# Performance work log

Measured on AMD Instinct MI355X. Metric: run time of the kernel, lower is better.

Reference implementation:

```python
import jax, jax.numpy as jnp
import numpy as np

C, H, V, N, T = 1024, 256, 10000, 16, 256


def setup_inputs() -> dict:
    key = jax.random.key(0)
    ks = jax.random.split(key, 16)
    s = 1.0 / np.sqrt(H)
    rn = lambda k, shape, sc: (jax.random.normal(k, shape, dtype=jnp.float32) * sc)
    d = {}
    d["text"] = jax.random.randint(ks[0], (N, T), 0, V)
    d["start_emb"] = rn(ks[1], (C, H), 1.0)
    d["sw1"] = rn(ks[2], (H, H), s); d["sb1"] = jnp.zeros((H,), jnp.float32)
    d["sw2"] = rn(ks[3], (H, H), s); d["sb2"] = jnp.zeros((H,), jnp.float32)
    d["sw3"] = rn(ks[4], (H, 1), s); d["sb3"] = jnp.zeros((1,), jnp.float32)
    d["state_emb"] = rn(ks[5], (C, H), 1.0)
    d["tw1"] = rn(ks[6], (H, H), s); d["tb1"] = jnp.zeros((H,), jnp.float32)
    d["tw2"] = rn(ks[7], (H, H), s); d["tb2"] = jnp.zeros((H,), jnp.float32)
    d["tw3"] = rn(ks[8], (H, C), s); d["tb3"] = jnp.zeros((C,), jnp.float32)
    d["pre_emb"] = rn(ks[9], (C, H), 1.0)
    d["ew1"] = rn(ks[10], (H, H), s); d["eb1"] = jnp.zeros((H,), jnp.float32)
    d["ew2"] = rn(ks[11], (H, H), s); d["eb2"] = jnp.zeros((H,), jnp.float32)
    d["ew3"] = rn(ks[12], (H, V), s); d["eb3"] = jnp.zeros((V,), jnp.float32)
    return d


def _res(x, w1, b1, w2, b2):
    # ResidualLayerOld: relu(lin2(relu(lin1(x)))) + x
    return jax.nn.relu(jax.nn.relu(x @ w1 + b1) @ w2 + b2) + x


def reference(text, start_emb, sw1, sb1, sw2, sb2, sw3, sb3,
              state_emb, tw1, tb1, tw2, tb2, tw3, tb3,
              pre_emb, ew1, eb1, ew2, eb2, ew3, eb3):
    # start: [C] log p(z_0)
    start = jax.nn.log_softmax((_res(start_emb, sw1, sb1, sw2, sb2) @ sw3 + sb3)[:, 0])
    # transition: log_softmax over next state, then permute -> [next, prev]
    trans = jax.nn.log_softmax(_res(state_emb, tw1, tb1, tw2, tb2) @ tw3 + tb3, axis=-1).T
    # emission: log_softmax over vocab, permute -> [V, C]
    emit = jax.nn.log_softmax(_res(pre_emb, ew1, eb1, ew2, eb2) @ ew3 + eb3, axis=-1).T

    obs = emit[text]                      # [N, T, C] log p(x_t | z_t=c)
    alpha0 = start[None, :] + obs[:, 0]   # [N, C]

    def step(alpha, e_t):
        # log-semiring matvec: alpha'[n,j] = logsumexp_i alpha[n,i] + trans[j,i]
        a = jax.scipy.special.logsumexp(alpha[:, None, :] + trans[None, :, :], axis=-1) + e_t
        return a, None

    alpha, _ = jax.lax.scan(step, alpha0, jnp.swapaxes(obs, 0, 1)[1:])
    # evidence: logsumexp over final states, summed over batch (full lengths)
    return jax.scipy.special.logsumexp(alpha, axis=-1).sum()
```

## Files before the change

### kernel.cpp

```cpp
#include <hip/hip_runtime.h>
#include <hip/hip_bf16.h>
#include <cstddef>

#define CC 1024
#define HH 256
#define VV 10000
#define NN 16
#define TT 256
#define NB 16
#define NVB 40

typedef __attribute__((ext_vector_type(8))) short s8b;
typedef __attribute__((ext_vector_type(4))) float f32x4;
typedef __attribute__((ext_vector_type(4))) unsigned int u32x4;

__device__ __forceinline__ unsigned short f2bf(float f) {
    unsigned int b = __builtin_bit_cast(unsigned int, f);
    b += 0x7FFFu + ((b >> 16) & 1u);
    return (unsigned short)(b >> 16);
}
__device__ __forceinline__ float bf2f(unsigned short u) {
    return __builtin_bit_cast(float, ((unsigned int)u) << 16);
}

struct ResArgs { const float *x, *w1, *b1, *w2, *b2; float* o; };
struct ResArgs3 { ResArgs a[3]; };

__global__ __launch_bounds__(256) void k_res(ResArgs3 A)
{
    ResArgs R = A.a[blockIdx.y];
    const int r0 = blockIdx.x * 16;
    const int th = threadIdx.x;
    __shared__ float xs[256][24];
    __shared__ float hs[256][24];
    #pragma unroll
    for (int k = 0; k < 16; k++) xs[th][k] = R.x[(size_t)(r0 + k) * HH + th];
    __syncthreads();
    float acc[16];
    float b1v = R.b1[th];
    #pragma unroll
    for (int r = 0; r < 16; r++) acc[r] = b1v;
    for (int h = 0; h < HH; h++) {
        float w = R.w1[(size_t)h * HH + th];
        #pragma unroll
        for (int r = 0; r < 16; r++) acc[r] = fmaf(xs[h][r], w, acc[r]);
    }
    #pragma unroll
    for (int r = 0; r < 16; r++) hs[th][r] = fmaxf(acc[r], 0.f);
    __syncthreads();
    float b2v = R.b2[th];
    #pragma unroll
    for (int r = 0; r < 16; r++) acc[r] = b2v;
    for (int h = 0; h < HH; h++) {
        float w = R.w2[(size_t)h * HH + th];
        #pragma unroll
        for (int r = 0; r < 16; r++) acc[r] = fmaf(hs[h][r], w, acc[r]);
    }
    #pragma unroll
    for (int r = 0; r < 16; r++) {
        size_t idx = (size_t)(r0 + r) * HH + th;
        R.o[idx] = fmaxf(acc[r], 0.f) + R.x[idx];
    }
}

__global__ __launch_bounds__(256) void k_slog(const float* __restrict__ res_s,
                                              const float* __restrict__ sw3,
                                              const float* __restrict__ sb3,
                                              float* __restrict__ slog)
{
    __shared__ float wv[256];
    const int th = threadIdx.x;
    const int c = blockIdx.x * 256 + th;
    wv[th] = sw3[th];
    __syncthreads();
    const float* row = res_s + (size_t)c * HH;
    float acc = 0.f;
    for (int h = 0; h < HH; h++) acc = fmaf(row[h], wv[h], acc);
    slog[c] = acc + sb3[0];
}

__global__ __launch_bounds__(256) void k_pt(const float* __restrict__ res_t,
                                            const float* __restrict__ tw3,
                                            const float* __restrict__ tb3,
                                            unsigned short* __restrict__ PB)
{
    const int r0 = blockIdx.x * 4;
    const int th = threadIdx.x;
    __shared__ float rs[4][256];
    __shared__ float sred[256];
    for (int k = 0; k < 4; k++) rs[k][th] = res_t[(size_t)(r0 + k) * HH + th];
    __syncthreads();
    float acc[4][4];
    #pragma unroll
    for (int r = 0; r < 4; r++)
        #pragma unroll
        for (int q = 0; q < 4; q++) acc[r][q] = tb3[th + q * 256];
    for (int h = 0; h < HH; h++) {
        float w0 = tw3[(size_t)h * CC + th];
        float w1 = tw3[(size_t)h * CC + th + 256];
        float w2 = tw3[(size_t)h * CC + th + 512];
        float w3 = tw3[(size_t)h * CC + th + 768];
        #pragma unroll
        for (int r = 0; r < 4; r++) {
            float xv = rs[r][h];
            acc[r][0] = fmaf(xv, w0, acc[r][0]);
            acc[r][1] = fmaf(xv, w1, acc[r][1]);
            acc[r][2] = fmaf(xv, w2, acc[r][2]);
            acc[r][3] = fmaf(xv, w3, acc[r][3]);
        }
    }
    for (int r = 0; r < 4; r++) {
        float m = fmaxf(fmaxf(acc[r][0], acc[r][1]), fmaxf(acc[r][2], acc[r][3]));
        sred[th] = m; __syncthreads();
        for (int off = 128; off > 0; off >>= 1) { if (th < off) sred[th] = fmaxf(sred[th], sred[th + off]); __syncthreads(); }
        float rm = sred[0]; __syncthreads();
        float ssum = __expf(acc[r][0] - rm) + __expf(acc[r][1] - rm) + __expf(acc[r][2] - rm) + __expf(acc[r][3] - rm);
        sred[th] = ssum; __syncthreads();
        for (int off = 128; off > 0; off >>= 1) { if (th < off) sred[th] += sred[th + off]; __syncthreads(); }
        float inv = 1.0f / sred[0]; __syncthreads();
        #pragma unroll
        for (int q = 0; q < 4; q++) {
            float p = __expf(acc[r][q] - rm) * inv;
            PB[(size_t)(th + q * 256) * CC + (r0 + r)] = f2bf(p);
        }
    }
}

__global__ __launch_bounds__(256) void k_emitg(const float* __restrict__ res_e,
                                               const float* __restrict__ ew3,
                                               const float* __restrict__ eb3,
                                               unsigned short* __restrict__ emitT,
                                               float* __restrict__ epart2)
{
    const int vb = blockIdx.x, c0 = blockIdx.y * 64;
    const int th = threadIdx.x;
    const int w = th >> 6, l = th & 63;
    const int lhi = l >> 4, llo = l & 15;
    const int wv = w & 1, wc = w >> 1;

    __shared__ __align__(16) unsigned short ewT[64 * 256];
    __shared__ __align__(16) unsigned short rsb[64 * 256];
    __shared__ float ebl[64];
    __shared__ float wlse[4][2][16][2];

    {
        char* base = (char*)rsb;
        #pragma unroll
        for (int i = 0; i < 8; i++) {
            int g = i * 2048 + th * 8;
            int row = g >> 8, h0 = g & 255;
            const float* src = res_e + (size_t)(c0 + row) * HH + h0;
            float4 f0 = *(const float4*)(src);
            float4 f1 = *(const float4*)(src + 4);
            s8b pk;
            pk[0] = (short)f2bf(f0.x); pk[1] = (short)f2bf(f0.y);
            pk[2] = (short)f2bf(f0.z); pk[3] = (short)f2bf(f0.w);
            pk[4] = (short)f2bf(f1.x); pk[5] = (short)f2bf(f1.y);
            pk[6] = (short)f2bf(f1.z); pk[7] = (short)f2bf(f1.w);
            *(s8b*)(base + row * 512 + ((h0 * 2) ^ ((row & 7) << 4))) = pk;
        }
    }

    float rM[2] = {-1e30f, -1e30f}, rS[2] = {0.f, 0.f};

    for (int r = 0; r < 4; r++) {
        const int v0r = vb * 256 + r * 64;
        __syncthreads();
        {
            int tv = th & 63;
            char* base = (char*)ewT;
            int rowoff = tv * 512;
            int key = (tv & 7) << 4;
            int vglob = v0r + tv;
            bool valid = vglob < VV;
            #pragma unroll 8
            for (int i = 0; i < 64; i++) {
                int h = (th >> 6) + i * 4;
                float x = valid ? ew3[(size_t)h * VV + vglob] : 0.f;
                *(unsigned short*)(base + rowoff + ((h * 2) ^ key)) = f2bf(x);
            }
        }
        if (th < 64) ebl[th] = (v0r + th < VV) ? eb3[v0r + th] : 0.f;
        __syncthreads();

        f32x4 acc[2][2] = {{{0,0,0,0},{0,0,0,0}},{{0,0,0,0},{0,0,0,0}}};
        const char* ea = (const char*)ewT;
        const char* rb = (const char*)rsb;
        const int arow0 = wv * 32 + llo, arow1 = wv * 32 + 16 + llo;
        const int brow0 = wc * 32 + llo, brow1 = wc * 32 + 16 + llo;
        const int akey0 = (arow0 & 7) << 4, akey1 = akey0;
        const int bkey0 = (brow0 & 7) << 4;
        #pragma unroll
        for (int kt = 0; kt < 8; kt++) {
            int off = kt * 64 + lhi * 16;
            s8b a0 = *(const s8b*)(ea + arow0 * 512 + (off ^ akey0));
            s8b a1 = *(const s8b*)(ea + arow1 * 512 + (off ^ akey1));
            s8b b0 = *(const s8b*)(rb + brow0 * 512 + (off ^ bkey0));
            s8b b1 = *(const s8b*)(rb + brow1 * 512 + (off ^ bkey0));
            acc[0][0] = __builtin_amdgcn_mfma_f32_16x16x32_bf16(a0, b0, acc[0][0], 0, 0, 0);
            acc[0][1] = __builtin_amdgcn_mfma_f32_16x16x32_bf16(a0, b1, acc[0][1], 0, 0, 0);
            acc[1][0] = __builtin_amdgcn_mfma_f32_16x16x32_bf16(a1, b0, acc[1][0], 0, 0, 0);
            acc[1][1] = __builtin_amdgcn_mfma_f32_16x16x32_bf16(a1, b1, acc[1][1], 0, 0, 0);
        }

        float um[2] = {-1e30f, -1e30f}, us[2] = {0.f, 0.f};
        #pragma unroll
        for (int u = 0; u < 2; u++) {
            float vals[8];
            #pragma unroll
            for (int s = 0; s < 2; s++) {
                #pragma unroll
                for (int q = 0; q < 4; q++) {
                    int vloc = wv * 32 + s * 16 + lhi * 4 + q;
                    int vglob = v0r + vloc;
                    float logit = acc[s][u][q] + ebl[vloc];
                    bool valid = vglob < VV;
                    if (valid)
                        emitT[(size_t)vglob * CC + (c0 + wc * 32 + u * 16 + llo)] = f2bf(logit);
                    vals[s * 4 + q] = valid ? logit : -1e30f;
                }
            }
            float m = vals[0];
            #pragma unroll
            for (int e = 1; e < 8; e++) m = fmaxf(m, vals[e]);
            float ss = 0.f;
            #pragma unroll
            for (int e = 0; e < 8; e++) ss += __expf(vals[e] - m);
            #pragma unroll
            for (int o = 16; o < 64; o <<= 1) {
                float m2 = __shfl_xor(m, o);
                float s2 = __shfl_xor(ss, o);
                float nm = fmaxf(m, m2);
                ss = ss * __expf(m - nm) + s2 * __expf(m2 - nm);
                m = nm;
            }
            um[u] = m; us[u] = ss;
        }
        if (l < 16) {
            #pragma unroll
            for (int u = 0; u < 2; u++) {
                wlse[w][u][l][0] = um[u];
                wlse[w][u][l][1] = us[u];
            }
        }
        __syncthreads();
        if (th < 64) {
            int wc2 = th >> 5, u2 = (th >> 4) & 1, ll2 = th & 15;
            float m1 = wlse[2 * wc2][u2][ll2][0], s1 = wlse[2 * wc2][u2][ll2][1];
            float m2 = wlse[2 * wc2 + 1][u2][ll2][0], s2 = wlse[2 * wc2 + 1][u2][ll2][1];
            float nm = fmaxf(m1, m2);
            float ns = s1 * __expf(m1 - nm) + s2 * __expf(m2 - nm);
            float om = rM[0], os = rS[0];
            float fm = fmaxf(om, nm);
            rS[0] = os * __expf(om - fm) + ns * __expf(nm - fm);
            rM[0] = fm;
        }
    }
    if (th < 64) {
        epart2[((size_t)vb * CC + c0 + th) * 2]     = rM[0];
        epart2[((size_t)vb * CC + c0 + th) * 2 + 1] = rS[0];
    }
}

__global__ __launch_bounds__(256) void k_lse(const float* __restrict__ epart2,
                                             float* __restrict__ lse)
{
    int c = blockIdx.x * 256 + threadIdx.x;
    float M = -1e30f, S = 0.f;
    for (int vb = 0; vb < NVB; vb++) {
        float m  = epart2[((size_t)vb * CC + c) * 2];
        float s2 = epart2[((size_t)vb * CC + c) * 2 + 1];
        float nm = fmaxf(M, m);
        S = S * __expf(M - nm) + s2 * __expf(m - nm);
        M = nm;
    }
    lse[c] = M + __logf(S);
}

__global__ __launch_bounds__(256) void k_eprob(unsigned short* __restrict__ emitT,
                                               const float* __restrict__ lse)
{
    __shared__ float ls[1024];
    const int th = threadIdx.x;
    for (int i = th; i < 1024; i += 256) ls[i] = lse[i];
    __syncthreads();
    size_t base = ((size_t)blockIdx.x * 256 + th) * 8;
    int c0 = (int)(base & 1023);
    s8b v = *(const s8b*)(emitT + base);
    unsigned short o[8];
    #pragma unroll
    for (int e = 0; e < 8; e++)
        o[e] = f2bf(__expf(bf2f((unsigned short)v[e]) - ls[c0 + e]));
    s8b ov;
    #pragma unroll
    for (int e = 0; e < 8; e++) ov[e] = (short)o[e];
    *(s8b*)(emitT + base) = ov;
}

__device__ __forceinline__ void load_stage(const unsigned short* vbuf_t, int th, char* vl)
{
    const unsigned short* sb = vbuf_t + th * 8;
    s8b ch[8];
    #pragma unroll
    for (int c = 0; c < 8; c++)
        asm volatile("global_load_dwordx4 %0, %1, off sc0 sc1"
                     : "=v"(ch[c]) : "v"(sb + c * 2048));
    asm volatile("s_waitcnt vmcnt(0)" ::: "memory");
    __builtin_amdgcn_sched_barrier(0);
    for (;;) {
        unsigned int miss = 0u;
        #pragma unroll
        for (int c = 0; c < 8; c++) {
            u32x4 d = __builtin_bit_cast(u32x4, ch[c]);
            if (d[0] == 0xFFFFFFFFu || d[1] == 0xFFFFFFFFu ||
                d[2] == 0xFFFFFFFFu || d[3] == 0xFFFFFFFFu) miss |= 1u << c;
        }
        if (miss == 0u) break;
        #pragma unroll
        for (int c = 0; c < 8; c++)
            if (miss & (1u << c))
                asm volatile("global_load_dwordx4 %0, %1, off sc0 sc1"
                             : "=v"(ch[c]) : "v"(sb + c * 2048));
        asm volatile("s_waitcnt vmcnt(0)" ::: "memory");
        __builtin_amdgcn_sched_barrier(0);
    }
    #pragma unroll
    for (int c = 0; c < 8; c++) {
        int ow = c * 4096 + th * 16;
        *(s8b*)(vl + (ow ^ (((ow >> 11) & 7) << 4))) = ch[c];
    }
}

__global__ void __launch_bounds__(256, 1) k_fwd(
    const unsigned short* __restrict__ PB,
    const unsigned short* __restrict__ eprob,
    const float* __restrict__ slog,
    const int* __restrict__ text,
    unsigned short* vbuf,
    float* __restrict__ outp)
{
    const int blk = blockIdx.x;
    const int th = threadIdx.x;
    const int w = th >> 6, l = th & 63;
    const int lhi = l >> 4, llo = l & 15;
    const int jglob = blk * 64 + w * 16 + llo;

    __shared__ int toks[NN * TT];
    __shared__ __align__(16) unsigned short vlds[NN * CC];
    __shared__ __align__(16) unsigned short vtile[16][72];
    __shared__ float swk[4];
    __shared__ float fin[16];

    for (int i = th; i < NN * TT; i += 256) toks[i] = text[i];

    s8b bfr[32];
    {
        const unsigned short* pbj = PB + (size_t)jglob * CC + lhi * 8;
        #pragma unroll
        for (int kt = 0; kt < 32; kt++)
            bfr[kt] = *(const s8b*)(pbj + kt * 32);
    }
    s8b ones;
    #pragma unroll
    for (int e = 0; e < 8; e++) ones[e] = (short)0x3F80;

    float x0 = slog[th], x1 = slog[th + 256], x2 = slog[th + 512], x3 = slog[th + 768];
    float mw = fmaxf(fmaxf(x0, x1), fmaxf(x2, x3));
    #pragma unroll
    for (int o = 32; o; o >>= 1) mw = fmaxf(mw, __shfl_xor(mw, o));
    __syncthreads();
    if (l == 0) swk[w] = mw;
    __syncthreads();
    float gm = fmaxf(fmaxf(swk[0], swk[1]), fmaxf(swk[2], swk[3]));
    __syncthreads();
    float e4 = __expf(x0 - gm) + __expf(x1 - gm) + __expf(x2 - gm) + __expf(x3 - gm);
    #pragma unroll
    for (int o = 32; o; o >>= 1) e4 += __shfl_xor(e4, o);
    if (l == 0) swk[w] = e4;
    __syncthreads();
    float slse = gm + __logf(swk[0] + swk[1] + swk[2] + swk[3]);
    __syncthreads();

    if (th < 64) {
        int jj = blk * 64 + th;
        float p0 = __expf(slog[jj] - slse);
        #pragma unroll
        for (int n = 0; n < 16; n++)
            vtile[n][th] = f2bf(p0 * bf2f(eprob[(size_t)toks[n * TT] * CC + jj]));
    }
    __syncthreads();
    if (th < 128) {
        int n = th >> 3, seg = th & 7;
        s8b val = *(const s8b*)&vtile[n][seg * 8];
        unsigned short* dst = vbuf + (size_t)n * CC + blk * 64 + seg * 8;
        asm volatile("global_store_dwordx4 %0, %1, off sc0 sc1" :: "v"(dst), "v"(val) : "memory");
    }

    float logaccq[4] = {0.f, 0.f, 0.f, 0.f};
    char* vl = (char*)vlds;
    const int rkey = (llo & 7) << 4;
    const int rbase = llo * 2048 + lhi * 16;

    for (int t = 1; t < TT; t++) {
        float epf[4];
        #pragma unroll
        for (int q = 0; q < 4; q++)
            epf[q] = bf2f(eprob[(size_t)toks[(lhi * 4 + q) * TT + t] * CC + jglob]);

        load_stage(vbuf + (size_t)(t - 1) * (NN * CC), th, vl);
        __syncthreads();

        f32x4 ac0 = {0,0,0,0}, ac1 = {0,0,0,0}, ac2 = {0,0,0,0}, ac3 = {0,0,0,0};
        f32x4 ao0 = {0,0,0,0}, ao1 = {0,0,0,0};
        #pragma unroll
        for (int kt = 0; kt < 32; kt += 4) {
            s8b a0 = *(const s8b*)(vl + ((rbase + (kt + 0) * 64) ^ rkey));
            s8b a1 = *(const s8b*)(vl + ((rbase + (kt + 1) * 64) ^ rkey));
            s8b a2 = *(const s8b*)(vl + ((rbase + (kt + 2) * 64) ^ rkey));
            s8b a3 = *(const s8b*)(vl + ((rbase + (kt + 3) * 64) ^ rkey));
            ac0 = __builtin_amdgcn_mfma_f32_16x16x32_bf16(a0, bfr[kt + 0], ac0, 0, 0, 0);
            ao0 = __builtin_amdgcn_mfma_f32_16x16x32_bf16(a0, ones,        ao0, 0, 0, 0);
            ac1 = __builtin_amdgcn_mfma_f32_16x16x32_bf16(a1, bfr[kt + 1], ac1, 0, 0, 0);
            ao1 = __builtin_amdgcn_mfma_f32_16x16x32_bf16(a1, ones,        ao1, 0, 0, 0);
            ac2 = __builtin_amdgcn_mfma_f32_16x16x32_bf16(a2, bfr[kt + 2], ac2, 0, 0, 0);
            ao0 = __builtin_amdgcn_mfma_f32_16x16x32_bf16(a2, ones,        ao0, 0, 0, 0);
            ac3 = __builtin_amdgcn_mfma_f32_16x16x32_bf16(a3, bfr[kt + 3], ac3, 0, 0, 0);
            ao1 = __builtin_amdgcn_mfma_f32_16x16x32_bf16(a3, ones,        ao1, 0, 0, 0);
        }
        f32x4 acc = (ac0 + ac1) + (ac2 + ac3);
        f32x4 aco = ao0 + ao1;

        #pragma unroll
        for (int q = 0; q < 4; q++) {
            float S = aco[q];
            logaccq[q] += __logf(S);
            float vq = acc[q] * (1.0f / S) * epf[q];
            vtile[lhi * 4 + q][w * 16 + llo] = f2bf(vq);
        }
        __syncthreads();

        if (th < 128) {
            int n = th >> 3, seg = th & 7;
            s8b val = *(const s8b*)&vtile[n][seg * 8];
            unsigned short* dst = vbuf + (size_t)t * (NN * CC) + (size_t)n * CC + blk * 64 + seg * 8;
            asm volatile("global_store_dwordx4 %0, %1, off sc0 sc1" :: "v"(dst), "v"(val) : "memory");
        }
    }

    if (blk == 0) {
        load_stage(vbuf + (size_t)255 * (NN * CC), th, vl);
        __syncthreads();
        f32x4 ao0 = {0,0,0,0}, ao1 = {0,0,0,0};
        #pragma unroll
        for (int kt = 0; kt < 32; kt += 2) {
            s8b a0 = *(const s8b*)(vl + ((rbase + (kt + 0) * 64) ^ rkey));
            s8b a1 = *(const s8b*)(vl + ((rbase + (kt + 1) * 64) ^ rkey));
            ao0 = __builtin_amdgcn_mfma_f32_16x16x32_bf16(a0, ones, ao0, 0, 0, 0);
            ao1 = __builtin_amdgcn_mfma_f32_16x16x32_bf16(a1, ones, ao1, 0, 0, 0);
        }
        f32x4 acoF = ao0 + ao1;
        if (w == 0 && llo == 0) {
            #pragma unroll
            for (int q = 0; q < 4; q++)
                fin[lhi * 4 + q] = logaccq[q] + __logf(acoF[q]);
        }
        __syncthreads();
        if (th == 0) {
            float tot = 0.f;
            for (int n = 0; n < 16; n++) tot += fin[n];
            outp[0] = tot;
        }
    }
}

extern "C" void kernel_launch(void* const* d_in, const int* in_sizes, int n_in,
                              void* d_out, int out_size, void* d_ws, size_t ws_size,
                              hipStream_t stream) {
    const int*   text      = (const int*)  d_in[0];
    const float* start_emb = (const float*)d_in[1];
    const float* sw1 = (const float*)d_in[2];
    const float* sb1 = (const float*)d_in[3];
    const float* sw2 = (const float*)d_in[4];
    const float* sb2 = (const float*)d_in[5];
    const float* sw3 = (const float*)d_in[6];
    const float* sb3 = (const float*)d_in[7];
    const float* state_emb = (const float*)d_in[8];
    const float* tw1 = (const float*)d_in[9];
    const float* tb1 = (const float*)d_in[10];
    const float* tw2 = (const float*)d_in[11];
    const float* tb2 = (const float*)d_in[12];
    const float* tw3 = (const float*)d_in[13];
    const float* tb3 = (const float*)d_in[14];
    const float* pre_emb = (const float*)d_in[15];
    const float* ew1 = (const float*)d_in[16];
    const float* eb1 = (const float*)d_in[17];
    const float* ew2 = (const float*)d_in[18];
    const float* eb2 = (const float*)d_in[19];
    const float* ew3 = (const float*)d_in[20];
    const float* eb3 = (const float*)d_in[21];

    char* wsp = (char*)d_ws;
    unsigned short* PB    = (unsigned short*)(wsp);
    unsigned short* emitT = (unsigned short*)(wsp + ((size_t)2 << 20));
    float* res_s = (float*)(wsp + ((size_t)2 << 20));
    float* res_t = (float*)(wsp + ((size_t)3 << 20));
    float* res_e = (float*)(wsp + 22577152u);
    float* slog  = (float*)(wsp + 23625728u);
    float* lse   = (float*)(wsp + 23629824u);
    float* epart2= (float*)(wsp + 23633920u);
    unsigned short* vbuf = (unsigned short*)(wsp + ((size_t)23 << 20));
    float* outp  = (float*)d_out;

    if (ws_size < ((size_t)31 << 20)) return;

    hipMemsetAsync(vbuf, 0xFF, (size_t)TT * NN * CC * sizeof(unsigned short), stream);

    ResArgs3 ra;
    ra.a[0] = { start_emb, sw1, sb1, sw2, sb2, res_s };
    ra.a[1] = { state_emb, tw1, tb1, tw2, tb2, res_t };
    ra.a[2] = { pre_emb,   ew1, eb1, ew2, eb2, res_e };

    hipLaunchKernelGGL(k_res,   dim3(64, 3),   dim3(256), 0, stream, ra);
    hipLaunchKernelGGL(k_slog,  dim3(4),       dim3(256), 0, stream, res_s, sw3, sb3, slog);
    hipLaunchKernelGGL(k_pt,    dim3(256),     dim3(256), 0, stream, res_t, tw3, tb3, PB);
    hipLaunchKernelGGL(k_emitg, dim3(NVB, 16), dim3(256), 0, stream, res_e, ew3, eb3, emitT, epart2);
    hipLaunchKernelGGL(k_lse,   dim3(4),       dim3(256), 0, stream, epart2, lse);
    hipLaunchKernelGGL(k_eprob, dim3(5000),    dim3(256), 0, stream, emitT, lse);
    hipLaunchKernelGGL(k_fwd,   dim3(NB),      dim3(256), 0, stream,
                       PB, emitT, slog, text, vbuf, outp);
}
```

Measured before the change: 979.3 us.

## Split forward recursion into half-batch phases with prefetch and fuse emission normalization

Removes the separate k_eprob pass and instead applies exp(logit - lse) lazily inside the forward kernel on the few gathered emission entries it needs. The forward scan now runs in two half-batch phases per timestep, prefetching the next phase's vbuf slice while MFMAs run on the current one, with separate log accumulators per half. This is meant to hide inter-block exchange latency on the serial critical path and to drop a full-size pass over emitT. The cost is twice as many barrier and spin rounds, plus extra exp work per step.

```diff
diff --git a/kernel.cpp b/kernel.cpp
--- a/kernel.cpp
+++ b/kernel.cpp
@@ -161,7 +161,7 @@
         }
     }
 
-    float rM[2] = {-1e30f, -1e30f}, rS[2] = {0.f, 0.f};
+    float rM = -1e30f, rS = 0.f;
 
     for (int r = 0; r < 4; r++) {
         const int v0r = vb * 256 + r * 64;
@@ -188,13 +188,13 @@
         const char* rb = (const char*)rsb;
         const int arow0 = wv * 32 + llo, arow1 = wv * 32 + 16 + llo;
         const int brow0 = wc * 32 + llo, brow1 = wc * 32 + 16 + llo;
-        const int akey0 = (arow0 & 7) << 4, akey1 = akey0;
+        const int akey0 = (arow0 & 7) << 4;
         const int bkey0 = (brow0 & 7) << 4;
         #pragma unroll
         for (int kt = 0; kt < 8; kt++) {
             int off = kt * 64 + lhi * 16;
             s8b a0 = *(const s8b*)(ea + arow0 * 512 + (off ^ akey0));
-            s8b a1 = *(const s8b*)(ea + arow1 * 512 + (off ^ akey1));
+            s8b a1 = *(const s8b*)(ea + arow1 * 512 + (off ^ akey0));
             s8b b0 = *(const s8b*)(rb + brow0 * 512 + (off ^ bkey0));
             s8b b1 = *(const s8b*)(rb + brow1 * 512 + (off ^ bkey0));
             acc[0][0] = __builtin_amdgcn_mfma_f32_16x16x32_bf16(a0, b0, acc[0][0], 0, 0, 0);
@@ -203,7 +203,7 @@
             acc[1][1] = __builtin_amdgcn_mfma_f32_16x16x32_bf16(a1, b1, acc[1][1], 0, 0, 0);
         }
 
-        float um[2] = {-1e30f, -1e30f}, us[2] = {0.f, 0.f};
+        float um[2], us[2];
         #pragma unroll
         for (int u = 0; u < 2; u++) {
             float vals[8];
@@ -250,15 +250,14 @@
             float m2 = wlse[2 * wc2 + 1][u2][ll2][0], s2 = wlse[2 * wc2 + 1][u2][ll2][1];
             float nm = fmaxf(m1, m2);
             float ns = s1 * __expf(m1 - nm) + s2 * __expf(m2 - nm);
-            float om = rM[0], os = rS[0];
-            float fm = fmaxf(om, nm);
-            rS[0] = os * __expf(om - fm) + ns * __expf(nm - fm);
-            rM[0] = fm;
+            float fm = fmaxf(rM, nm);
+            rS = rS * __expf(rM - fm) + ns * __expf(nm - fm);
+            rM = fm;
         }
     }
     if (th < 64) {
-        epart2[((size_t)vb * CC + c0 + th) * 2]     = rM[0];
-        epart2[((size_t)vb * CC + c0 + th) * 2 + 1] = rS[0];
+        epart2[((size_t)vb * CC + c0 + th) * 2]     = rM;
+        epart2[((size_t)vb * CC + c0 + th) * 2 + 1] = rS;
     }
 }
 
@@ -277,27 +276,7 @@
     lse[c] = M + __logf(S);
 }
 
-__global__ __launch_bounds__(256) void k_eprob(unsigned short* __restrict__ emitT,
-                                               const float* __restrict__ lse)
-{
-    __shared__ float ls[1024];
-    const int th = threadIdx.x;
-    for (int i = th; i < 1024; i += 256) ls[i] = lse[i];
-    __syncthreads();
-    size_t base = ((size_t)blockIdx.x * 256 + th) * 8;
-    int c0 = (int)(base & 1023);
-    s8b v = *(const s8b*)(emitT + base);
-    unsigned short o[8];
-    #pragma unroll
-    for (int e = 0; e < 8; e++)
-        o[e] = f2bf(__expf(bf2f((unsigned short)v[e]) - ls[c0 + e]));
-    s8b ov;
-    #pragma unroll
-    for (int e = 0; e < 8; e++) ov[e] = (short)o[e];
-    *(s8b*)(emitT + base) = ov;
-}
-
-__device__ __forceinline__ void load_stage(const unsigned short* vbuf_t, int th, char* vl)
+__device__ __forceinline__ void load_stage_full(const unsigned short* vbuf_t, int th, char* vl)
 {
     const unsigned short* sb = vbuf_t + th * 8;
     s8b ch[8];
@@ -315,7 +294,7 @@
             if (d[0] == 0xFFFFFFFFu || d[1] == 0xFFFFFFFFu ||
                 d[2] == 0xFFFFFFFFu || d[3] == 0xFFFFFFFFu) miss |= 1u << c;
         }
-        if (miss == 0u) break;
+        if (!__any(miss != 0u)) break;
         #pragma unroll
         for (int c = 0; c < 8; c++)
             if (miss & (1u << c))
@@ -333,7 +312,8 @@
 
 __global__ void __launch_bounds__(256, 1) k_fwd(
     const unsigned short* __restrict__ PB,
-    const unsigned short* __restrict__ eprob,
+    const unsigned short* __restrict__ emitT,
+    const float* __restrict__ lse,
     const float* __restrict__ slog,
     const int* __restrict__ text,
     unsigned short* vbuf,
@@ -349,6 +329,7 @@
     __shared__ __align__(16) unsigned short vlds[NN * CC];
     __shared__ __align__(16) unsigned short vtile[16][72];
     __shared__ float swk[4];
+    __shared__ float sfin[16];
     __shared__ float fin[16];
 
     for (int i = th; i < NN * TT; i += 256) toks[i] = text[i];
@@ -364,6 +345,8 @@
     #pragma unroll
     for (int e = 0; e < 8; e++) ones[e] = (short)0x3F80;
 
+    const float lse_j = lse[jglob];
+
     float x0 = slog[th], x1 = slog[th + 256], x2 = slog[th + 512], x3 = slog[th + 768];
     float mw = fmaxf(fmaxf(x0, x1), fmaxf(x2, x3));
     #pragma unroll
@@ -384,9 +367,10 @@
     if (th < 64) {
         int jj = blk * 64 + th;
         float p0 = __expf(slog[jj] - slse);
+        float lsej = lse[jj];
         #pragma unroll
         for (int n = 0; n < 16; n++)
-            vtile[n][th] = f2bf(p0 * bf2f(eprob[(size_t)toks[n * TT] * CC + jj]));
+            vtile[n][th] = f2bf(p0 * __expf(bf2f(emitT[(size_t)toks[n * TT] * CC + jj]) - lsej));
     }
     __syncthreads();
     if (th < 128) {
@@ -396,20 +380,70 @@
         asm volatile("global_store_dwordx4 %0, %1, off sc0 sc1" :: "v"(dst), "v"(val) : "memory");
     }
 
-    float logaccq[4] = {0.f, 0.f, 0.f, 0.f};
+    s8b pend[4];
+    {
+        const unsigned short* pb = vbuf + th * 8;
+        #pragma unroll
+        for (int c = 0; c < 4; c++)
+            asm volatile("global_load_dwordx4 %0, %1, off sc0 sc1"
+                         : "=v"(pend[c]) : "v"(pb + c * 2048));
+    }
+
+    float logA[4] = {0,0,0,0}, logB[4] = {0,0,0,0};
     char* vl = (char*)vlds;
     const int rkey = (llo & 7) << 4;
-    const int rbase = llo * 2048 + lhi * 16;
-
-    for (int t = 1; t < TT; t++) {
-        float epf[4];
-        #pragma unroll
-        for (int q = 0; q < 4; q++)
-            epf[q] = bf2f(eprob[(size_t)toks[(lhi * 4 + q) * TT + t] * CC + jglob]);
-
-        load_stage(vbuf + (size_t)(t - 1) * (NN * CC), th, vl);
-        __syncthreads();
-
+
+    for (int ph = 0; ph < 510; ph++) {
+        const int g = ph & 1, t = (ph >> 1) + 1, slot = t - 1;
+
+        asm volatile("s_waitcnt vmcnt(0)" ::: "memory");
+        __builtin_amdgcn_sched_barrier(0);
+        {
+            const unsigned short* pb = vbuf + (size_t)slot * (NN * CC) + g * 8192 + th * 8;
+            for (;;) {
+                unsigned int miss = 0u;
+                #pragma unroll
+                for (int c = 0; c < 4; c++) {
+                    u32x4 d = __builtin_bit_cast(u32x4, pend[c]);
+                    if (d[0] == 0xFFFFFFFFu || d[1] == 0xFFFFFFFFu ||
+                        d[2] == 0xFFFFFFFFu || d[3] == 0xFFFFFFFFu) miss |= 1u << c;
+                }
+                if (!__any(miss != 0u)) break;
+                #pragma unroll
+                for (int c = 0; c < 4; c++)
+                    if (miss & (1u << c))
+                        asm volatile("global_load_dwordx4 %0, %1, off sc0 sc1"
+                                     : "=v"(pend[c]) : "v"(pb + c * 2048));
+                asm volatile("s_waitcnt vmcnt(0)" ::: "memory");
+                __builtin_amdgcn_sched_barrier(0);
+            }
+        }
+
+        #pragma unroll
+        for (int c = 0; c < 4; c++) {
+            int ow = g * 16384 + th * 16 + c * 4096;
+            *(s8b*)(vl + (ow ^ (((ow >> 11) & 7) << 4))) = pend[c];
+        }
+
+        unsigned int epfu[4];
+        #pragma unroll
+        for (int q = 0; q < 4; q++) {
+            int r = (lhi * 4 + q) & 7;
+            const unsigned short* ep = emitT + (size_t)toks[(g * 8 + r) * TT + t] * CC + jglob;
+            asm volatile("global_load_ushort %0, %1, off" : "=v"(epfu[q]) : "v"(ep));
+        }
+        __syncthreads();
+
+        if (ph < 509) {
+            const int g2 = (ph + 1) & 1, s2 = (ph + 1) >> 1;
+            const unsigned short* pb2 = vbuf + (size_t)s2 * (NN * CC) + g2 * 8192 + th * 8;
+            #pragma unroll
+            for (int c = 0; c < 4; c++)
+                asm volatile("global_load_dwordx4 %0, %1, off sc0 sc1"
+                             : "=v"(pend[c]) : "v"(pb2 + c * 2048));
+        }
+
+        const int rbase = (g * 8 + (llo & 7)) * 2048 + lhi * 16;
         f32x4 ac0 = {0,0,0,0}, ac1 = {0,0,0,0}, ac2 = {0,0,0,0}, ac3 = {0,0,0,0};
         f32x4 ao0 = {0,0,0,0}, ao1 = {0,0,0,0};
         #pragma unroll
@@ -430,39 +464,57 @@
         f32x4 acc = (ac0 + ac1) + (ac2 + ac3);
         f32x4 aco = ao0 + ao1;
 
-        #pragma unroll
-        for (int q = 0; q < 4; q++) {
-            float S = aco[q];
-            logaccq[q] += __logf(S);
-            float vq = acc[q] * (1.0f / S) * epf[q];
-            vtile[lhi * 4 + q][w * 16 + llo] = f2bf(vq);
-        }
-        __syncthreads();
-
-        if (th < 128) {
+        if (ph < 509) { asm volatile("s_waitcnt vmcnt(4)" ::: "memory"); }
+        else          { asm volatile("s_waitcnt vmcnt(0)" ::: "memory"); }
+        __builtin_amdgcn_sched_barrier(0);
+
+        if (lhi < 2) {
+            #pragma unroll
+            for (int q = 0; q < 4; q++) {
+                int r = lhi * 4 + q;
+                float S = aco[q];
+                float lg = __logf(S);
+                if (g == 0) logA[q] += lg; else logB[q] += lg;
+                float ep = __expf(bf2f((unsigned short)epfu[q]) - lse_j);
+                float vq = acc[q] * (1.0f / S) * ep;
+                vtile[r][w * 16 + llo] = f2bf(vq);
+            }
+        }
+        __syncthreads();
+
+        if (th < 64) {
             int n = th >> 3, seg = th & 7;
             s8b val = *(const s8b*)&vtile[n][seg * 8];
-            unsigned short* dst = vbuf + (size_t)t * (NN * CC) + (size_t)n * CC + blk * 64 + seg * 8;
+            unsigned short* dst = vbuf + (size_t)t * (NN * CC) + (size_t)(g * 8 + n) * CC + blk * 64 + seg * 8;
             asm volatile("global_store_dwordx4 %0, %1, off sc0 sc1" :: "v"(dst), "v"(val) : "memory");
         }
     }
 
     if (blk == 0) {
-        load_stage(vbuf + (size_t)255 * (NN * CC), th, vl);
-        __syncthreads();
-        f32x4 ao0 = {0,0,0,0}, ao1 = {0,0,0,0};
+        load_stage_full(vbuf + (size_t)255 * (NN * CC), th, vl);
+        __syncthreads();
+        const int rbaseF = llo * 2048 + lhi * 16;
+        f32x4 fo0 = {0,0,0,0}, fo1 = {0,0,0,0};
         #pragma unroll
         for (int kt = 0; kt < 32; kt += 2) {
-            s8b a0 = *(const s8b*)(vl + ((rbase + (kt + 0) * 64) ^ rkey));
-            s8b a1 = *(const s8b*)(vl + ((rbase + (kt + 1) * 64) ^ rkey));
-            ao0 = __builtin_amdgcn_mfma_f32_16x16x32_bf16(a0, ones, ao0, 0, 0, 0);
-            ao1 = __builtin_amdgcn_mfma_f32_16x16x32_bf16(a1, ones, ao1, 0, 0, 0);
-        }
-        f32x4 acoF = ao0 + ao1;
+            s8b a0 = *(const s8b*)(vl + ((rbaseF + (kt + 0) * 64) ^ rkey));
+            s8b a1 = *(const s8b*)(vl + ((rbaseF + (kt + 1) * 64) ^ rkey));
+            fo0 = __builtin_amdgcn_mfma_f32_16x16x32_bf16(a0, ones, fo0, 0, 0, 0);
+            fo1 = __builtin_amdgcn_mfma_f32_16x16x32_bf16(a1, ones, fo1, 0, 0, 0);
+        }
+        f32x4 acoF = fo0 + fo1;
         if (w == 0 && llo == 0) {
             #pragma unroll
-            for (int q = 0; q < 4; q++)
-                fin[lhi * 4 + q] = logaccq[q] + __logf(acoF[q]);
+            for (int q = 0; q < 4; q++) sfin[lhi * 4 + q] = acoF[q];
+        }
+        __syncthreads();
+        if (w == 0 && llo == 0 && lhi < 2) {
+            #pragma unroll
+            for (int q = 0; q < 4; q++) {
+                int r = lhi * 4 + q;
+                fin[r]     = logA[q] + __logf(sfin[r]);
+                fin[8 + r] = logB[q] + __logf(sfin[8 + r]);
+            }
         }
         __syncthreads();
         if (th == 0) {
@@ -525,7 +577,6 @@
     hipLaunchKernelGGL(k_pt,    dim3(256),     dim3(256), 0, stream, res_t, tw3, tb3, PB);
     hipLaunchKernelGGL(k_emitg, dim3(NVB, 16), dim3(256), 0, stream, res_e, ew3, eb3, emitT, epart2);
     hipLaunchKernelGGL(k_lse,   dim3(4),       dim3(256), 0, stream, epart2, lse);
-    hipLaunchKernelGGL(k_eprob, dim3(5000),    dim3(256), 0, stream, emitT, lse);
     hipLaunchKernelGGL(k_fwd,   dim3(NB),      dim3(256), 0, stream,
-                       PB, emitT, slog, text, vbuf, outp);
-}
+                       PB, emitT, lse, slog, text, vbuf, outp);
+}
```

Result: slower. 1.292 ms (+31.9%).
